# Optimization experiments

Measured on AMD Instinct MI355X. Metric: run time of the kernel, lower is better.

## Reference

```python
import jax, jax.numpy as jnp
import numpy as np

B, D_IN, D_H = 4096, 1024, 1024


def setup_inputs() -> dict:
    key = jax.random.key(0)
    ks = jax.random.split(key, 11)
    s = 1.0 / np.sqrt(D_IN + D_H)  # torch Linear default init scale
    inp = {
        "x": jax.random.normal(ks[0], (B, D_IN), jnp.float32),
        "h": jax.random.normal(ks[1], (B, D_H), jnp.float32),
        "c": jax.random.normal(ks[2], (B, D_H), jnp.float32),
        "W_f": jax.random.uniform(ks[3], (D_IN + D_H, D_H), jnp.float32, -s, s),
        "b_f": jax.random.uniform(ks[4], (D_H,), jnp.float32, -s, s),
        "W_i": jax.random.uniform(ks[5], (D_IN + D_H, D_H), jnp.float32, -s, s),
        "b_i": jax.random.uniform(ks[6], (D_H,), jnp.float32, -s, s),
        "W_c": jax.random.uniform(ks[7], (D_IN + D_H, D_H), jnp.float32, -s, s),
        "b_c": jax.random.uniform(ks[8], (D_H,), jnp.float32, -s, s),
        "W_o": jax.random.uniform(ks[9], (D_IN + D_H, D_H), jnp.float32, -s, s),
        "b_o": jax.random.uniform(ks[10], (D_H,), jnp.float32, -s, s),
    }
    return inp


def reference(x, h, c, W_f, b_f, W_i, b_i, W_c, b_c, W_o, b_o):
    xh = jnp.concatenate([x, h], axis=1)  # [B, D_IN+D_H]
    # fuse four gate linears into one GEMM: [B, 2H] @ [2H, 4H]
    W = jnp.concatenate([W_f, W_i, W_c, W_o], axis=1)
    b = jnp.concatenate([b_f, b_i, b_c, b_o], axis=0)
    gates = xh @ W + b  # [B, 4H]
    f_g, i_g, c_g, o_g = jnp.split(gates, 4, axis=1)
    f = jax.nn.sigmoid(f_g)
    i = jax.nn.sigmoid(i_g)
    ct = jnp.tanh(c_g)
    ot = jax.nn.sigmoid(o_g)
    c_new = f * c + i * ct
    h_new = ot * jnp.tanh(c_new)
    return (h_new, (h_new, c_new))
```

## Files before the change

### kernel.cpp

```cpp
#include <hip/hip_runtime.h>
#include <hip/hip_bf16.h>
#include <cstdint>

typedef __bf16 bf16x8 __attribute__((ext_vector_type(8)));
typedef float f32x4 __attribute__((ext_vector_type(4)));

#define BROWS 4096
#define DH    1024
#define KDIM  2048
#define NT    32

__global__ __launch_bounds__(256) void k_prep(const float* __restrict__ x,
                                              const float* __restrict__ h,
                                              const float* __restrict__ Wf,
                                              const float* __restrict__ Wi,
                                              const float* __restrict__ Wc,
                                              const float* __restrict__ Wo,
                                              __hip_bfloat16* __restrict__ xh,
                                              __hip_bfloat16* __restrict__ wt) {
  __shared__ float t[64][65];
  const int tid = threadIdx.x;
  if (blockIdx.x < 4096) {
    int64_t idx = ((int64_t)blockIdx.x * 256 + tid) * 8;
    int row = (int)(idx >> 11);
    int col = (int)(idx & 2047);
    const float* src = (col < 1024) ? (x + (int64_t)row * 1024 + col)
                                    : (h + (int64_t)row * 1024 + (col - 1024));
    float4 v0 = reinterpret_cast<const float4*>(src)[0];
    float4 v1 = reinterpret_cast<const float4*>(src)[1];
    alignas(16) __hip_bfloat16 o8[8];
    o8[0] = __float2bfloat16(v0.x); o8[1] = __float2bfloat16(v0.y);
    o8[2] = __float2bfloat16(v0.z); o8[3] = __float2bfloat16(v0.w);
    o8[4] = __float2bfloat16(v1.x); o8[5] = __float2bfloat16(v1.y);
    o8[6] = __float2bfloat16(v1.z); o8[7] = __float2bfloat16(v1.w);
    *reinterpret_cast<int4*>(xh + idx) = *reinterpret_cast<const int4*>(o8);
  } else {
    const int b = blockIdx.x - 4096;
    const int g  = b & 3;
    const int jt = (b >> 2) & 15;
    const int kt = b >> 6;
    const float* W = (g == 0) ? Wf : (g == 1) ? Wi : (g == 2) ? Wc : Wo;
    const int j0 = jt << 6, k0 = kt << 6;
#pragma unroll
    for (int i = 0; i < 4; ++i) {
      int r = (tid >> 4) + (i << 4);
      int c = (tid & 15) << 2;
      float4 v = *reinterpret_cast<const float4*>(W + (int64_t)(k0 + r) * 1024 + j0 + c);
      t[r][c + 0] = v.x; t[r][c + 1] = v.y; t[r][c + 2] = v.z; t[r][c + 3] = v.w;
    }
    __syncthreads();
#pragma unroll
    for (int i = 0; i < 2; ++i) {
      int task = tid + (i << 8);
      int rr = task >> 3;
      int kc = (task & 7) << 3;
      int np = (((jt << 2) + (rr >> 4)) << 6) + (g << 4) + (rr & 15);
      alignas(16) __hip_bfloat16 o8[8];
#pragma unroll
      for (int e = 0; e < 8; ++e) o8[e] = __float2bfloat16(t[kc + e][rr]);
      *reinterpret_cast<int4*>(wt + (int64_t)np * KDIM + k0 + kc) =
          *reinterpret_cast<const int4*>(o8);
    }
  }
}

__device__ __forceinline__ float sig_(float v) {
  return __builtin_amdgcn_rcpf(1.0f + __expf(-v));
}
__device__ __forceinline__ float tanh_(float v) {
  return fmaf(2.0f, __builtin_amdgcn_rcpf(1.0f + __expf(-2.0f * v)), -1.0f);
}

#define GLD(PTR, LOFF)                                                           \
  __builtin_amdgcn_global_load_lds(                                              \
      (const __attribute__((address_space(1))) void*)(PTR),                      \
      (__attribute__((address_space(3))) void*)(lds + (LOFF) + wslot), 16, 0, 0)

#define STG2(LP, KH_, PA, PB)                                                    \
  do {                                                                           \
    GLD((PA), (LP) + (KH_) * 8192);                                              \
    GLD((PA) + 128 * KDIM, (LP) + (KH_) * 8192 + 4096);                          \
    GLD((PB), (LP) + 16384 + (KH_) * 8192);                                      \
    GLD((PB) + 128 * KDIM, (LP) + 16384 + (KH_) * 8192 + 4096);                  \
  } while (0)

#define VM4 asm volatile("s_waitcnt vmcnt(4)" ::: "memory")
#define SB0 __builtin_amdgcn_sched_barrier(0)
#define LGKM4 asm volatile("s_waitcnt lgkmcnt(4)" ::: "memory")
#define LGKM8 asm volatile("s_waitcnt lgkmcnt(8)" ::: "memory")

#define DSR(DST, ABASE, OFF)                                                     \
  asm volatile("ds_read_b128 %0, %1 offset:%2"                                   \
               : "=&v"(DST) : "v"(ABASE), "i"(OFF))

#define RD_AV(BANK, AB, KH, H)                                                   \
  do {                                                                           \
    DSR(BANK[0], AB, (KH) * 16384 + ((H) * 4 + 0) * 1024);                       \
    DSR(BANK[1], AB, (KH) * 16384 + ((H) * 4 + 1) * 1024);                       \
    DSR(BANK[2], AB, (KH) * 16384 + ((H) * 4 + 2) * 1024);                       \
    DSR(BANK[3], AB, (KH) * 16384 + ((H) * 4 + 3) * 1024);                       \
  } while (0)
#define RD_BV(BANK, BB, KH)                                                      \
  do {                                                                           \
    DSR(BANK[0], BB, (KH) * 16384 + 0 * 1024);                                   \
    DSR(BANK[1], BB, (KH) * 16384 + 1 * 1024);                                   \
    DSR(BANK[2], BB, (KH) * 16384 + 2 * 1024);                                   \
    DSR(BANK[3], BB, (KH) * 16384 + 3 * 1024);                                   \
  } while (0)

#define MM(BA, BB, MIH_, LG)                                                     \
  do {                                                                           \
    LG; SB0;                                                                     \
    __builtin_amdgcn_s_setprio(1);                                               \
    _Pragma("unroll") for (int i = 0; i < 4; ++i)                                \
      _Pragma("unroll") for (int ni = 0; ni < 4; ++ni)                           \
        acc[(MIH_) * 4 + i][ni] = __builtin_amdgcn_mfma_f32_16x16x32_bf16(       \
            BA[i], BB[ni], acc[(MIH_) * 4 + i][ni], 0, 0, 0);                    \
    __builtin_amdgcn_s_setprio(0);                                               \
    __builtin_amdgcn_s_barrier();                                                \
  } while (0)

#define ADV do { a0 += 64; b0 += 64; } while (0)

__global__ __launch_bounds__(512, 2) void k_lstm_gemm(
    const __hip_bfloat16* __restrict__ xh, const __hip_bfloat16* __restrict__ wt,
    const float* __restrict__ cin,
    const float* __restrict__ bfp, const float* __restrict__ bip,
    const float* __restrict__ bcp, const float* __restrict__ bop,
    float* __restrict__ out) {
  __shared__ __hip_bfloat16 lds[65536];
  const int tid  = threadIdx.x;
  const int lane = tid & 63;
  const int wid  = tid >> 6;
  const int wm = wid >> 2, wn = wid & 3;
  const int wmb = wm << 7, wnb = wn << 6;

  const int bid  = blockIdx.x;
  const int flat = ((bid & 7) << 5) | (bid >> 3);
  const int m0 = (flat & 15) << 8;
  const int n0 = (flat >> 4) << 8;

  f32x4 acc[8][4] = {};

  const int wslot = wid << 9;
  const int cl = (((lane & 3) ^ ((lane >> 3) & 3)) << 3);
  const __hip_bfloat16* a0 = xh + (int64_t)(m0 + (tid >> 2)) * KDIM + cl;
  const __hip_bfloat16* b0 = wt + (int64_t)(n0 + (tid >> 2)) * KDIM + cl;

  const int frow = lane & 15;
  const int rx   = (((lane >> 4) ^ ((frow >> 1) & 3)) << 3);
  const int aA0 = ((((wmb + frow) << 5) + rx) << 1);
  const int aA1 = aA0 + 65536;
  const int bB0 = (((16384 + ((wnb + frow) << 5) + rx)) << 1);
  const int bB1 = bB0 + 65536;

  bf16x8 avA[4], avB[4], bvA[4], bvB[4];

  STG2(0, 0, a0, b0);
  STG2(0, 1, a0 + 32, b0 + 32);
  ADV;
  VM4;
  __builtin_amdgcn_s_barrier();
  RD_AV(avA, aA0, 0, 0);
  RD_BV(bvA, bB0, 0);

  for (int t = 0; t < NT; t += 2) {
    {
      RD_AV(avB, aA0, 0, 1);
      STG2(32768, 0, a0, b0);
      VM4; MM(avA, bvA, 0, LGKM4);
      RD_AV(avA, aA0, 1, 0); RD_BV(bvB, bB0, 1);
      STG2(32768, 1, a0 + 32, b0 + 32);
      MM(avB, bvA, 1, LGKM8);
      RD_AV(avB, aA0, 1, 1);
      VM4; MM(avA, bvB, 0, LGKM4);
      RD_AV(avA, aA1, 0, 0); RD_BV(bvA, bB1, 0);
      MM(avB, bvB, 1, LGKM8);
    }
    if (t != 30) ADV;
    {
      RD_AV(avB, aA1, 0, 1);
      STG2(0, 0, a0, b0);
      VM4; MM(avA, bvA, 0, LGKM4);
      RD_AV(avA, aA1, 1, 0); RD_BV(bvB, bB1, 1);
      STG2(0, 1, a0 + 32, b0 + 32);
      MM(avB, bvA, 1, LGKM8);
      RD_AV(avB, aA1, 1, 1);
      VM4; MM(avA, bvB, 0, LGKM4);
      RD_AV(avA, aA0, 0, 0); RD_BV(bvA, bB0, 0);
      MM(avB, bvB, 1, LGKM8);
    }
    ADV;
  }
  asm volatile("s_waitcnt lgkmcnt(0)" ::: "memory");

  const int j = (((n0 >> 6) + wn) << 4) + frow;
  const float vbf = bfp[j], vbi = bip[j], vbc = bcp[j], vbo = bop[j];
  const int q4 = (lane >> 4) << 2;
  float* outh1 = out;
  float* outh2 = out + (int64_t)BROWS * DH;
  float* outc  = out + (int64_t)2 * BROWS * DH;
#pragma unroll
  for (int mi = 0; mi < 8; ++mi) {
    const int mbase = m0 + wmb + (mi << 4) + q4;
#pragma unroll
    for (int r = 0; r < 4; ++r) {
      const int m = mbase + r;
      const int64_t idx = (int64_t)m * DH + j;
      float fg = sig_(acc[mi][0][r] + vbf);
      float ig = sig_(acc[mi][1][r] + vbi);
      float cg = tanh_(acc[mi][2][r] + vbc);
      float og = sig_(acc[mi][3][r] + vbo);
      float cn = fg * cin[idx] + ig * cg;
      float hn = og * tanh_(cn);
      outh1[idx] = hn;
      outh2[idx] = hn;
      outc[idx]  = cn;
    }
  }
}

extern "C" void kernel_launch(void* const* d_in, const int* in_sizes, int n_in,
                              void* d_out, int out_size, void* d_ws, size_t ws_size,
                              hipStream_t stream) {
  const float* x  = (const float*)d_in[0];
  const float* h  = (const float*)d_in[1];
  const float* c  = (const float*)d_in[2];
  const float* Wf = (const float*)d_in[3];
  const float* bf = (const float*)d_in[4];
  const float* Wi = (const float*)d_in[5];
  const float* bi = (const float*)d_in[6];
  const float* Wc = (const float*)d_in[7];
  const float* bc = (const float*)d_in[8];
  const float* Wo = (const float*)d_in[9];
  const float* bo = (const float*)d_in[10];
  float* out = (float*)d_out;

  __hip_bfloat16* xh = (__hip_bfloat16*)d_ws;
  __hip_bfloat16* wt = xh + (int64_t)BROWS * KDIM;

  hipLaunchKernelGGL(k_prep, dim3(6144), dim3(256), 0, stream,
                     x, h, Wf, Wi, Wc, Wo, xh, wt);
  hipLaunchKernelGGL(k_lstm_gemm, dim3(256), dim3(512), 0, stream,
                     xh, wt, c, bf, bi, bc, bo, out);
}
```

Before: 87.77 us.

## Restructure GEMM main loop into per-half tiles with fewer barriers

Replaces the software-pipelined main loop, which prefetched LDS fragments for the next sub-step across MFMA groups and placed a barrier after every MFMA group, with a simpler TILE macro. Each K-half now issues all LDS reads for that half, launches the global-to-LDS loads for the next stage, runs two MFMA groups, and then waits once and places a single barrier. This cuts the number of workgroup barriers per iteration from four to two. In exchange, LDS reads are no longer overlapped with the previous half's MFMAs, so LDS latency may be more exposed.

Measured after the change: 86.94 us. About the same (-0.9%).

```diff
diff --git a/kernel.cpp b/kernel.cpp
--- a/kernel.cpp
+++ b/kernel.cpp
@@ -76,18 +76,14 @@
       (const __attribute__((address_space(1))) void*)(PTR),                      \
       (__attribute__((address_space(3))) void*)(lds + (LOFF) + wslot), 16, 0, 0)
 
-#define STG2(LP, KH_, PA, PB)                                                    \
-  do {                                                                           \
-    GLD((PA), (LP) + (KH_) * 8192);                                              \
-    GLD((PA) + 128 * KDIM, (LP) + (KH_) * 8192 + 4096);                          \
-    GLD((PB), (LP) + 16384 + (KH_) * 8192);                                      \
-    GLD((PB) + 128 * KDIM, (LP) + 16384 + (KH_) * 8192 + 4096);                  \
-  } while (0)
+#define STGA(PTR, LOFF)                                                          \
+  do { GLD((PTR), (LOFF)); GLD((PTR) + 128 * KDIM, (LOFF) + 4096); } while (0)
 
 #define VM4 asm volatile("s_waitcnt vmcnt(4)" ::: "memory")
+#define LG4 asm volatile("s_waitcnt lgkmcnt(4)" ::: "memory")
+#define LG0 asm volatile("s_waitcnt lgkmcnt(0)" ::: "memory")
 #define SB0 __builtin_amdgcn_sched_barrier(0)
-#define LGKM4 asm volatile("s_waitcnt lgkmcnt(4)" ::: "memory")
-#define LGKM8 asm volatile("s_waitcnt lgkmcnt(8)" ::: "memory")
+#define BAR __builtin_amdgcn_s_barrier()
 
 #define DSR(DST, ABASE, OFF)                                                     \
   asm volatile("ds_read_b128 %0, %1 offset:%2"                                   \
@@ -108,16 +104,32 @@
     DSR(BANK[3], BB, (KH) * 16384 + 3 * 1024);                                   \
   } while (0)
 
-#define MM(BA, BB, MIH_, LG)                                                     \
-  do {                                                                           \
-    LG; SB0;                                                                     \
+#define MM(BA, BB, H)                                                            \
+  do {                                                                           \
     __builtin_amdgcn_s_setprio(1);                                               \
     _Pragma("unroll") for (int i = 0; i < 4; ++i)                                \
       _Pragma("unroll") for (int ni = 0; ni < 4; ++ni)                           \
-        acc[(MIH_) * 4 + i][ni] = __builtin_amdgcn_mfma_f32_16x16x32_bf16(       \
-            BA[i], BB[ni], acc[(MIH_) * 4 + i][ni], 0, 0, 0);                    \
+        acc[(H) * 4 + i][ni] = __builtin_amdgcn_mfma_f32_16x16x32_bf16(          \
+            BA[i], BB[ni], acc[(H) * 4 + i][ni], 0, 0, 0);                       \
     __builtin_amdgcn_s_setprio(0);                                               \
-    __builtin_amdgcn_s_barrier();                                                \
+  } while (0)
+
+#define TILE(AB, BB, SLP)                                                        \
+  do {                                                                           \
+    RD_AV(avA, AB, 0, 0);                                                        \
+    RD_BV(bvA, BB, 0);                                                           \
+    RD_AV(avB, AB, 0, 1);                                                        \
+    STGA(a0, SLP); STGA(b0, (SLP) + 16384);                                      \
+    LG4; SB0; MM(avA, bvA, 0);                                                   \
+    LG0; SB0; MM(avB, bvA, 1);                                                   \
+    VM4; BAR;       \
+    RD_AV(avA, AB, 1, 0);                                                        \
+    RD_BV(bvB, BB, 1);                                                           \
+    RD_AV(avB, AB, 1, 1);                                                        \
+    STGA(a0 + 32, (SLP) + 8192); STGA(b0 + 32, (SLP) + 16384 + 8192);            \
+    LG4; SB0; MM(avA, bvB, 0);                                                   \
+    LG0; SB0; MM(avB, bvB, 1);                                                   \
+    VM4; BAR;     \
   } while (0)
 
 #define ADV do { a0 += 64; b0 += 64; } while (0)
@@ -156,43 +168,21 @@
 
   bf16x8 avA[4], avB[4], bvA[4], bvB[4];
 
-  STG2(0, 0, a0, b0);
-  STG2(0, 1, a0 + 32, b0 + 32);
+  STGA(a0, 0);
+  STGA(b0, 16384);
+  STGA(a0 + 32, 8192);
+  STGA(b0 + 32, 16384 + 8192);
   ADV;
   VM4;
-  __builtin_amdgcn_s_barrier();
-  RD_AV(avA, aA0, 0, 0);
-  RD_BV(bvA, bB0, 0);
+  BAR;
 
   for (int t = 0; t < NT; t += 2) {
-    {
-      RD_AV(avB, aA0, 0, 1);
-      STG2(32768, 0, a0, b0);
-      VM4; MM(avA, bvA, 0, LGKM4);
-      RD_AV(avA, aA0, 1, 0); RD_BV(bvB, bB0, 1);
-      STG2(32768, 1, a0 + 32, b0 + 32);
-      MM(avB, bvA, 1, LGKM8);
-      RD_AV(avB, aA0, 1, 1);
-      VM4; MM(avA, bvB, 0, LGKM4);
-      RD_AV(avA, aA1, 0, 0); RD_BV(bvA, bB1, 0);
-      MM(avB, bvB, 1, LGKM8);
-    }
+    TILE(aA0, bB0, 32768);
     if (t != 30) ADV;
-    {
-      RD_AV(avB, aA1, 0, 1);
-      STG2(0, 0, a0, b0);
-      VM4; MM(avA, bvA, 0, LGKM4);
-      RD_AV(avA, aA1, 1, 0); RD_BV(bvB, bB1, 1);
-      STG2(0, 1, a0 + 32, b0 + 32);
-      MM(avB, bvA, 1, LGKM8);
-      RD_AV(avB, aA1, 1, 1);
-      VM4; MM(avA, bvB, 0, LGKM4);
-      RD_AV(avA, aA0, 0, 0); RD_BV(bvA, bB0, 0);
-      MM(avB, bvB, 1, LGKM8);
-    }
+    TILE(aA1, bB1, 0);
     ADV;
   }
-  asm volatile("s_waitcnt lgkmcnt(0)" ::: "memory");
+  LG0;
 
   const int j = (((n0 >> 6) + wn) << 4) + frow;
   const float vbf = bfp[j], vbi = bip[j], vbc = bcp[j], vbo = bop[j];
```
